# Kernel optimization log

Measured on AMD Instinct MI355X. Metric: run time of the kernel, lower is better.

Reference implementation:

```python
import jax, jax.numpy as jnp
import numpy as np
from jax import lax

Q = 512   # number of FSA states
S = 64    # alphabet size
B = 64    # batch of sequences
T = 256   # sequence length (fixed / padded)


def setup_inputs() -> dict:
    key = jax.random.key(0)
    k_a, k_i, k_f, k_x = jax.random.split(key, 4)
    # Log-space weights centered at -log(Q) so exp(A) ~ 1/Q and the real-semiring
    # forward recursion stays numerically O(1) over T steps.
    A = (-jnp.log(Q) + 0.01 * jax.random.normal(k_a, (Q, S, Q))).astype(jnp.float32)
    init = (-jnp.log(Q) + 0.01 * jax.random.normal(k_i, (Q,))).astype(jnp.float32)
    final = (0.01 * jax.random.normal(k_f, (Q,))).astype(jnp.float32)
    xs = jax.random.randint(k_x, (B, T), 0, S, dtype=jnp.int32)
    return {"A": A, "init": init, "final": final, "xs": xs}


def reference(A, init, final, xs):
    # Weighted-FSA forward algorithm in the real semiring.
    # A: log-space transition weights (Q, S, Q); exp -> positive weights.
    # alpha_t[q] = sum_{q'} exp(A)[q, x_t, q'] * alpha_{t-1}[q']
    A_exp = jnp.exp(A)                       # (Q, S, Q)
    A_sym = jnp.transpose(A_exp, (1, 0, 2))  # (S, Q, Q) for symbol-indexed gather
    b = xs.shape[0]
    alpha0 = jnp.broadcast_to(jnp.exp(init), (b, A.shape[0]))  # (B, Q)

    def step(alpha, x_t):
        # x_t: (B,) symbols at this timestep; gather per-symbol transition matrices
        A_x = A_sym[x_t]                                  # (B, Q, Q)
        alpha = jnp.einsum('bij,bj->bi', A_x, alpha)      # batched matvec
        return alpha, None

    alpha_T, _ = lax.scan(step, alpha0, xs.T)  # scan over time: xs.T is (T, B)
    # Terminate with final weights, return per-sequence log-likelihood (B,)
    return jnp.log(alpha_T @ jnp.exp(final))
```

## Files before the change

### kernel.cpp

```cpp
#include <hip/hip_runtime.h>

#define QN 512
#define SN 64
#define BN 64
#define TN 256
#define GS 4

typedef unsigned long long ull;

#if defined(__has_builtin)
#if __has_builtin(__builtin_amdgcn_sdot4)
#define SDOT4(a, b, c) __builtin_amdgcn_sdot4((a), (b), (c), false)
#endif
#endif
#ifndef SDOT4
static __device__ __forceinline__ int sdot4_sw(int a, int b, int c) {
    c += (int)(signed char)(a)       * (int)(signed char)(b);
    c += (int)(signed char)(a >> 8)  * (int)(signed char)(b >> 8);
    c += (int)(signed char)(a >> 16) * (int)(signed char)(b >> 16);
    c += (int)(signed char)(a >> 24) * (int)(signed char)(b >> 24);
    return c;
}
#define SDOT4(a, b, c) sdot4_sw((a), (b), (c))
#endif

#define NIB_LO(x) ((((x) & 0x0F0F0F0F) ^ 0x08080808) - 0x08080808)
#define NIB_HI(x) (((((x) >> 4) & 0x0F0F0F0F) ^ 0x08080808) - 0x08080808)

static __device__ __forceinline__ float wave_sum(float v) {
    #pragma unroll
    for (int o = 32; o > 0; o >>= 1) v += __shfl_xor(v, o, 64);
    return v;
}
static __device__ __forceinline__ float wave_max(float v) {
    #pragma unroll
    for (int o = 32; o > 0; o >>= 1) v = fmaxf(v, __shfl_xor(v, o, 64));
    return v;
}

static __device__ __forceinline__ void barrier_lds(void) {
    __builtin_amdgcn_s_waitcnt(0xC07F);
    __builtin_amdgcn_s_barrier();
}

static __device__ __forceinline__ void st_tag(ull* p, ull v) {
    __hip_atomic_store(p, v, __ATOMIC_RELAXED, __HIP_MEMORY_SCOPE_AGENT);
}
static __device__ __forceinline__ ull ld_tag(const ull* p) {
    return __hip_atomic_load(p, __ATOMIC_RELAXED, __HIP_MEMORY_SCOPE_AGENT);
}

#define POLL_GUARD (1 << 20)

__global__ __launch_bounds__(256) void k_minmax(const float* __restrict__ A,
                                                unsigned* __restrict__ smax) {
    const int s  = blockIdx.x >> 3;
    const int i0 = (blockIdx.x & 7) * 64;
    const int tl = threadIdx.x & 127;
    const int rh = threadIdx.x >> 7;
    float mx = -1e30f, mn = 1e30f;
    for (int ro = 0; ro < 64; ro += 2) {
        const int i = i0 + ro + rh;
        float4 a4 = ((const float4*)A)[(size_t)(i * 64 + s) * 128 + tl];
        mx = fmaxf(mx, fmaxf(fmaxf(a4.x, a4.y), fmaxf(a4.z, a4.w)));
        mn = fminf(mn, fminf(fminf(a4.x, a4.y), fminf(a4.z, a4.w)));
    }
    mx = wave_max(mx);
    mn = -wave_max(-mn);
    if ((threadIdx.x & 63) == 0) {
        const float c = 1.0f / 512.0f;
        float se = fmaxf(expf(mx) - c, c - expf(mn));
        atomicMax(&smax[s], __float_as_uint(se));
    }
}

__global__ __launch_bounds__(256) void k_quant(const float* __restrict__ A,
                                               const unsigned* __restrict__ smax,
                                               int* __restrict__ Epk,
                                               float* __restrict__ ES,
                                               float* __restrict__ CS) {
    __shared__ int tile[64][129];
    __shared__ float fsumC[64][4];
    const int s  = blockIdx.x >> 3;
    const int i0 = (blockIdx.x & 7) * 64;
    const float se  = __uint_as_float(smax[s]);
    const float inv = se > 0.0f ? 7.0f / se : 0.0f;
    const float c = 1.0f / 512.0f;
    const int tl = threadIdx.x & 127;
    const int rh = threadIdx.x >> 7;
    if (threadIdx.x < 256) ((float*)fsumC)[threadIdx.x] = 0.0f;
    __syncthreads();
    for (int ro = 0; ro < 64; ro += 2) {
        const int r = ro + rh;
        const int i = i0 + r;
        float4 a4 = ((const float4*)A)[(size_t)(i * 64 + s) * 128 + tl];
        const float e0 = expf(a4.x) - c, e1 = expf(a4.y) - c;
        const float e2 = expf(a4.z) - c, e3 = expf(a4.w) - c;
        int q0 = (int)rintf(fminf(fmaxf(e0 * inv, -7.0f), 7.0f));
        int q1 = (int)rintf(fminf(fmaxf(e1 * inv, -7.0f), 7.0f));
        int q2 = (int)rintf(fminf(fmaxf(e2 * inv, -7.0f), 7.0f));
        int q3 = (int)rintf(fminf(fmaxf(e3 * inv, -7.0f), 7.0f));
        tile[r][tl] = (q0 & 255) | ((q1 & 255) << 8) | ((q2 & 255) << 16) | ((q3 & 255) << 24);
        float gs = e0 + e1 + e2 + e3;
        #pragma unroll
        for (int o = 16; o > 0; o >>= 1) gs += __shfl_xor(gs, o, 64);
        if ((threadIdx.x & 31) == 0) atomicAdd(&fsumC[r][tl >> 5], gs);
    }
    __syncthreads();
    if (threadIdx.x < 256) {
        const int r = threadIdx.x >> 2, gg = threadIdx.x & 3;
        CS[((size_t)(s * GS + gg) << 9) + i0 + r] = fsumC[r][gg];
    }
    if (threadIdx.x < 64) {
        const int r = threadIdx.x;
        ES[(s << 9) + i0 + r] = (fsumC[r][0] + fsumC[r][1]) + (fsumC[r][2] + fsumC[r][3]);
    }
    const int il = threadIdx.x & 63;
    const int jg = threadIdx.x >> 6;
    for (int jo = 0; jo < 4; ++jo) {
        const int j32 = jg * 4 + jo;
        int4 v;
        v.x = (tile[il][8 * j32 + 0] & 0x0F0F0F0F) | ((tile[il][8 * j32 + 4] & 0x0F0F0F0F) << 4);
        v.y = (tile[il][8 * j32 + 1] & 0x0F0F0F0F) | ((tile[il][8 * j32 + 5] & 0x0F0F0F0F) << 4);
        v.z = (tile[il][8 * j32 + 2] & 0x0F0F0F0F) | ((tile[il][8 * j32 + 6] & 0x0F0F0F0F) << 4);
        v.w = (tile[il][8 * j32 + 3] & 0x0F0F0F0F) | ((tile[il][8 * j32 + 7] & 0x0F0F0F0F) << 4);
        ((int4*)Epk)[((size_t)(s * 16 + j32) * 512) + i0 + il] = v;
    }
}

__global__ __launch_bounds__(1024) void k_fsa(const int* __restrict__ Epk,
                                              const float* __restrict__ ES,
                                              const float* __restrict__ CS,
                                              const unsigned* __restrict__ smax,
                                              const float* __restrict__ init_w,
                                              const float* __restrict__ fin_w,
                                              const int* __restrict__ xs,
                                              ull* __restrict__ ax,
                                              float* __restrict__ out) {
    __shared__ __align__(16) int qa[2][QN / 4];
    __shared__ __align__(16) int qloc[QN / 16];
    __shared__ int   xs_l[TN];
    __shared__ float wsum[8];
    __shared__ float sws[8];
    __shared__ float se_l[SN];
    __shared__ float mb[2];

    const int t    = threadIdx.x;
    const int b    = blockIdx.x & (BN - 1);
    const int g    = blockIdx.x >> 6;
    const int lane = t & 63, wave = t >> 6;
    const int tr   = t & 3;
    const int lr   = t >> 2;
    const int irow = (g << 7) + lr;
    const int u    = t - 512;

    if (t < TN) xs_l[t] = xs[b * TN + t];
    if (t < SN) se_l[t] = __uint_as_float(smax[t]) * (0.125f / 889.0f);

    const float c  = 1.0f / 512.0f;
    const float Kq = 0.125f;

    const int4* __restrict__ Epb = (const int4*)Epk;
    int4 eR[4], eC[4];
    float ESv = 0.0f, CSv = 0.0f;
    float av = 0.0f;

    if (t < 512) {
        const int s0 = xs[b * TN], s1 = xs[b * TN + 1];
        const int4* EpR = Epb + (size_t)(s0 * 16 + tr * 4) * 512 + irow;
        const int4* EpC = Epb + (size_t)(s1 * 16 + g * 4) * 512 + t;
        #pragma unroll
        for (int k = 0; k < 4; ++k) { eR[k] = EpR[(size_t)k * 512]; eC[k] = EpC[(size_t)k * 512]; }
        if (tr == 0) ESv = ES[(s0 << 9) + irow];
        CSv = CS[((size_t)(s1 * GS + g) << 9) + t];
    } else {
        av = expf(init_w[u]);
        float ws = wave_sum(av);
        if (lane == 0) wsum[wave - 8] = ws;
    }
    barrier_lds();
    if (t >= 512) {
        float m0 = 0.0f;
        #pragma unroll
        for (int w = 0; w < 8; ++w) m0 += wsum[w];
        const float mu     = m0 * (1.0f / 512.0f);
        const float inv_sa = 127.0f / (Kq * mu);
        const int q = (int)rintf(fminf(fmaxf((av - mu) * inv_sa, -127.0f), 127.0f));
        ((char*)qa)[u] = (char)q;
        if (u == 0) mb[0] = m0;
    }
    barrier_lds();

    for (int k = 0; k < TN / 2; ++k) {
        const int par = k & 1;
        float mu = 0.0f;
        if (t < 512) {
            const int sR  = xs_l[2 * k];
            const int sRn = xs_l[(2 * k + 2) & (TN - 1)];
            const float mm = mb[par];
            mu = mm * (1.0f / 512.0f);
            const int4* qp   = (const int4*)qa[par];
            const int4* EpRn = Epb + (size_t)(sRn * 16 + tr * 4) * 512 + irow;
            int a0 = 0, a1 = 0, a2 = 0, a3 = 0;
            #pragma unroll
            for (int k4 = 0; k4 < 4; ++k4) {
                const int4 E4 = eR[k4];
                eR[k4] = EpRn[(size_t)k4 * 512];
                const int4 qlo = qp[2 * (4 * tr + k4) + 0];
                const int4 qhi = qp[2 * (4 * tr + k4) + 1];
                a0 = SDOT4(NIB_LO(E4.x), qlo.x, a0);
                a1 = SDOT4(NIB_HI(E4.x), qhi.x, a1);
                a2 = SDOT4(NIB_LO(E4.y), qlo.y, a2);
                a3 = SDOT4(NIB_HI(E4.y), qhi.y, a3);
                a0 = SDOT4(NIB_LO(E4.z), qlo.z, a0);
                a1 = SDOT4(NIB_HI(E4.z), qhi.z, a1);
                a2 = SDOT4(NIB_LO(E4.w), qlo.w, a2);
                a3 = SDOT4(NIB_HI(E4.w), qhi.w, a3);
            }
            __builtin_amdgcn_sched_barrier(0);
            int acc = (a0 + a1) + (a2 + a3);
            acc += __shfl_xor(acc, 1, 64);
            acc += __shfl_xor(acc, 2, 64);
            float outv = 0.0f;
            if (tr == 0) {
                outv = c * mm + mu * (ESv + se_l[sR] * (float)acc);
                ESv = ES[(sRn << 9) + irow];
                const float inv_sa = 127.0f / (Kq * mu);
                const int q8 = (int)rintf(fminf(fmaxf((outv - mu) * inv_sa, -127.0f), 127.0f));
                ((char*)qloc)[lr] = (char)q8;
            }
            float ws = wave_sum(outv);
            if (lane == 0) sws[wave] = ws;
        }
        barrier_lds();

        if (t < 512) {
            const int sC  = xs_l[2 * k + 1];
            const int sCn = xs_l[(2 * k + 3) & (TN - 1)];
            float Sg = 0.0f;
            #pragma unroll
            for (int w = 0; w < 8; ++w) Sg += sws[w];
            const int4* qc   = (const int4*)qloc;
            const int4* EpCn = Epb + (size_t)(sCn * 16 + g * 4) * 512 + t;
            int a0 = 0, a1 = 0, a2 = 0, a3 = 0;
            #pragma unroll
            for (int k4 = 0; k4 < 4; ++k4) {
                const int4 E4 = eC[k4];
                eC[k4] = EpCn[(size_t)k4 * 512];
                const int4 ql = qc[2 * k4 + 0];
                const int4 qh = qc[2 * k4 + 1];
                a0 = SDOT4(NIB_LO(E4.x), ql.x, a0);
                a1 = SDOT4(NIB_HI(E4.x), qh.x, a1);
                a2 = SDOT4(NIB_LO(E4.y), ql.y, a2);
                a3 = SDOT4(NIB_HI(E4.y), qh.y, a3);
                a0 = SDOT4(NIB_LO(E4.z), ql.z, a0);
                a1 = SDOT4(NIB_HI(E4.z), qh.z, a1);
                a2 = SDOT4(NIB_LO(E4.w), ql.w, a2);
                a3 = SDOT4(NIB_HI(E4.w), qh.w, a3);
            }
            __builtin_amdgcn_sched_barrier(0);
            const int accC = (a0 + a1) + (a2 + a3);
            const float y = c * Sg + mu * (CSv + se_l[sC] * (float)accC);
            CSv = CS[((size_t)(sCn * GS + g) << 9) + t];
            st_tag(ax + ((size_t)((par ^ 1) * BN + b) * GS + g) * QN + t,
                   ((ull)(unsigned)(k + 1) << 32) | (ull)__float_as_uint(y));
        } else {
            const unsigned want = (unsigned)(k + 1);
            const ull* ap = ax + (size_t)((par ^ 1) * BN + b) * GS * QN + u;
            ull w0 = ld_tag(ap + 0 * QN);
            ull w1 = ld_tag(ap + 1 * QN);
            ull w2 = ld_tag(ap + 2 * QN);
            ull w3 = ld_tag(ap + 3 * QN);
            int gd = 0;
            while ((((unsigned)(w0 >> 32) < want) | ((unsigned)(w1 >> 32) < want) |
                    ((unsigned)(w2 >> 32) < want) | ((unsigned)(w3 >> 32) < want)) &&
                   ++gd < POLL_GUARD) {
                __builtin_amdgcn_s_sleep(1);
                w0 = ld_tag(ap + 0 * QN);
                w1 = ld_tag(ap + 1 * QN);
                w2 = ld_tag(ap + 2 * QN);
                w3 = ld_tag(ap + 3 * QN);
            }
            av = (__uint_as_float((unsigned)w0) + __uint_as_float((unsigned)w1)) +
                 (__uint_as_float((unsigned)w2) + __uint_as_float((unsigned)w3));
            float ws = wave_sum(av);
            if (lane == 0) wsum[wave - 8] = ws;
        }
        barrier_lds();

        if (t >= 512) {
            float m = 0.0f;
            #pragma unroll
            for (int w = 0; w < 8; ++w) m += wsum[w];
            const float mu2    = m * (1.0f / 512.0f);
            const float inv_sa = 127.0f / (Kq * mu2);
            const int q = (int)rintf(fminf(fmaxf((av - mu2) * inv_sa, -127.0f), 127.0f));
            ((char*)qa)[(par ^ 1) * QN + u] = (char)q;
            if (u == 0) mb[par ^ 1] = m;
        }
        barrier_lds();
    }

    {
        float v = 0.0f;
        if (t >= 512) {
            v = av * expf(fin_w[u]);
            float ws = wave_sum(v);
            if (lane == 0) wsum[wave - 8] = ws;
        }
        barrier_lds();
        if (g == 0 && t == 512) {
            float tot = 0.0f;
            #pragma unroll
            for (int w = 0; w < 8; ++w) tot += wsum[w];
            out[b] = logf(tot);
        }
    }
}

extern "C" void kernel_launch(void* const* d_in, const int* in_sizes, int n_in,
                              void* d_out, int out_size, void* d_ws, size_t ws_size,
                              hipStream_t stream) {
    const float* A      = (const float*)d_in[0];
    const float* init_w = (const float*)d_in[1];
    const float* fin_w  = (const float*)d_in[2];
    const int*   xs     = (const int*)d_in[3];
    float* out = (float*)d_out;

    char* ws = (char*)d_ws;
    int*      Epk  = (int*)ws;
    float*    ES   = (float*)(ws + (8u << 20));
    float*    CS   = (float*)(ws + (8u << 20) + (128u << 10));
    unsigned* smax = (unsigned*)(ws + (8u << 20) + (640u << 10));
    ull*      ax   = (ull*)(ws + (8u << 20) + (641u << 10));

    hipMemsetAsync(smax, 0, (1u << 10) + (2u << 20), stream);
    k_minmax<<<512, 256, 0, stream>>>(A, smax);
    k_quant<<<512, 256, 0, stream>>>(A, smax, Epk, ES, CS);
    k_fsa<<<GS * BN, 1024, 0, stream>>>(Epk, ES, CS, smax, init_w, fin_w, xs, ax, out);
}
```

Measured before the change: 651.7 us.

## Split each sequence's FSA recursion across eight workgroups instead of four

Doubles the number of cooperating workgroups per sequence (GS 4→8), so each block handles 64 rows and a 64-column slice of the quantized transition matrix. This halves the per-block register preload and the dot-product work per step. In exchange, each step now needs eight tagged partial vectors to be polled and summed, an extra shuffle stage is added, and twice as many blocks (512) must be co-resident for the inter-block spin synchronization to make progress. Workspace offsets and the memset size are enlarged to fit the larger partial-sum buffer.

```diff
diff --git a/kernel.cpp b/kernel.cpp
--- a/kernel.cpp
+++ b/kernel.cpp
@@ -4,7 +4,7 @@
 #define SN 64
 #define BN 64
 #define TN 256
-#define GS 4
+#define GS 8
 
 typedef unsigned long long ull;
 
@@ -80,7 +80,7 @@
                                                float* __restrict__ ES,
                                                float* __restrict__ CS) {
     __shared__ int tile[64][129];
-    __shared__ float fsumC[64][4];
+    __shared__ float fsumC[64][GS];
     const int s  = blockIdx.x >> 3;
     const int i0 = (blockIdx.x & 7) * 64;
     const float se  = __uint_as_float(smax[s]);
@@ -88,7 +88,10 @@
     const float c = 1.0f / 512.0f;
     const int tl = threadIdx.x & 127;
     const int rh = threadIdx.x >> 7;
-    if (threadIdx.x < 256) ((float*)fsumC)[threadIdx.x] = 0.0f;
+    if (threadIdx.x < 256) {
+        ((float*)fsumC)[threadIdx.x] = 0.0f;
+        ((float*)fsumC)[256 + threadIdx.x] = 0.0f;
+    }
     __syncthreads();
     for (int ro = 0; ro < 64; ro += 2) {
         const int r = ro + rh;
@@ -103,17 +106,24 @@
         tile[r][tl] = (q0 & 255) | ((q1 & 255) << 8) | ((q2 & 255) << 16) | ((q3 & 255) << 24);
         float gs = e0 + e1 + e2 + e3;
         #pragma unroll
-        for (int o = 16; o > 0; o >>= 1) gs += __shfl_xor(gs, o, 64);
-        if ((threadIdx.x & 31) == 0) atomicAdd(&fsumC[r][tl >> 5], gs);
+        for (int o = 8; o > 0; o >>= 1) gs += __shfl_xor(gs, o, 64);
+        if ((threadIdx.x & 15) == 0) atomicAdd(&fsumC[r][tl >> 4], gs);
     }
     __syncthreads();
     if (threadIdx.x < 256) {
-        const int r = threadIdx.x >> 2, gg = threadIdx.x & 3;
-        CS[((size_t)(s * GS + gg) << 9) + i0 + r] = fsumC[r][gg];
+        #pragma unroll
+        for (int h = 0; h < 2; ++h) {
+            const int idx = threadIdx.x + 256 * h;
+            const int r = idx >> 3, gg = idx & 7;
+            CS[((size_t)(s * GS + gg) << 9) + i0 + r] = fsumC[r][gg];
+        }
     }
     if (threadIdx.x < 64) {
         const int r = threadIdx.x;
-        ES[(s << 9) + i0 + r] = (fsumC[r][0] + fsumC[r][1]) + (fsumC[r][2] + fsumC[r][3]);
+        float es = 0.0f;
+        #pragma unroll
+        for (int gg = 0; gg < GS; ++gg) es += fsumC[r][gg];
+        ES[(s << 9) + i0 + r] = es;
     }
     const int il = threadIdx.x & 63;
     const int jg = threadIdx.x >> 6;
@@ -128,17 +138,17 @@
     }
 }
 
-__global__ __launch_bounds__(1024) void k_fsa(const int* __restrict__ Epk,
-                                              const float* __restrict__ ES,
-                                              const float* __restrict__ CS,
-                                              const unsigned* __restrict__ smax,
-                                              const float* __restrict__ init_w,
-                                              const float* __restrict__ fin_w,
-                                              const int* __restrict__ xs,
-                                              ull* __restrict__ ax,
-                                              float* __restrict__ out) {
+__global__ __launch_bounds__(1024, 8) void k_fsa(const int* __restrict__ Epk,
+                                                 const float* __restrict__ ES,
+                                                 const float* __restrict__ CS,
+                                                 const unsigned* __restrict__ smax,
+                                                 const float* __restrict__ init_w,
+                                                 const float* __restrict__ fin_w,
+                                                 const int* __restrict__ xs,
+                                                 ull* __restrict__ ax,
+                                                 float* __restrict__ out) {
     __shared__ __align__(16) int qa[2][QN / 4];
-    __shared__ __align__(16) int qloc[QN / 16];
+    __shared__ __align__(16) int qloc[16];
     __shared__ int   xs_l[TN];
     __shared__ float wsum[8];
     __shared__ float sws[8];
@@ -149,9 +159,9 @@
     const int b    = blockIdx.x & (BN - 1);
     const int g    = blockIdx.x >> 6;
     const int lane = t & 63, wave = t >> 6;
-    const int tr   = t & 3;
-    const int lr   = t >> 2;
-    const int irow = (g << 7) + lr;
+    const int tr   = t & 7;
+    const int lr   = t >> 3;
+    const int irow = (g << 6) + lr;
     const int u    = t - 512;
 
     if (t < TN) xs_l[t] = xs[b * TN + t];
@@ -161,16 +171,16 @@
     const float Kq = 0.125f;
 
     const int4* __restrict__ Epb = (const int4*)Epk;
-    int4 eR[4], eC[4];
+    int4 eR[2], eC[2];
     float ESv = 0.0f, CSv = 0.0f;
     float av = 0.0f;
 
     if (t < 512) {
         const int s0 = xs[b * TN], s1 = xs[b * TN + 1];
-        const int4* EpR = Epb + (size_t)(s0 * 16 + tr * 4) * 512 + irow;
-        const int4* EpC = Epb + (size_t)(s1 * 16 + g * 4) * 512 + t;
-        #pragma unroll
-        for (int k = 0; k < 4; ++k) { eR[k] = EpR[(size_t)k * 512]; eC[k] = EpC[(size_t)k * 512]; }
+        const int4* EpR = Epb + (size_t)(s0 * 16 + tr * 2) * 512 + irow;
+        const int4* EpC = Epb + (size_t)(s1 * 16 + g * 2) * 512 + t;
+        #pragma unroll
+        for (int k = 0; k < 2; ++k) { eR[k] = EpR[(size_t)k * 512]; eC[k] = EpC[(size_t)k * 512]; }
         if (tr == 0) ESv = ES[(s0 << 9) + irow];
         CSv = CS[((size_t)(s1 * GS + g) << 9) + t];
     } else {
@@ -200,14 +210,14 @@
             const float mm = mb[par];
             mu = mm * (1.0f / 512.0f);
             const int4* qp   = (const int4*)qa[par];
-            const int4* EpRn = Epb + (size_t)(sRn * 16 + tr * 4) * 512 + irow;
+            const int4* EpRn = Epb + (size_t)(sRn * 16 + tr * 2) * 512 + irow;
             int a0 = 0, a1 = 0, a2 = 0, a3 = 0;
             #pragma unroll
-            for (int k4 = 0; k4 < 4; ++k4) {
+            for (int k4 = 0; k4 < 2; ++k4) {
                 const int4 E4 = eR[k4];
                 eR[k4] = EpRn[(size_t)k4 * 512];
-                const int4 qlo = qp[2 * (4 * tr + k4) + 0];
-                const int4 qhi = qp[2 * (4 * tr + k4) + 1];
+                const int4 qlo = qp[2 * (2 * tr + k4) + 0];
+                const int4 qhi = qp[2 * (2 * tr + k4) + 1];
                 a0 = SDOT4(NIB_LO(E4.x), qlo.x, a0);
                 a1 = SDOT4(NIB_HI(E4.x), qhi.x, a1);
                 a2 = SDOT4(NIB_LO(E4.y), qlo.y, a2);
@@ -221,6 +231,7 @@
             int acc = (a0 + a1) + (a2 + a3);
             acc += __shfl_xor(acc, 1, 64);
             acc += __shfl_xor(acc, 2, 64);
+            acc += __shfl_xor(acc, 4, 64);
             float outv = 0.0f;
             if (tr == 0) {
                 outv = c * mm + mu * (ESv + se_l[sR] * (float)acc);
@@ -241,10 +252,10 @@
             #pragma unroll
             for (int w = 0; w < 8; ++w) Sg += sws[w];
             const int4* qc   = (const int4*)qloc;
-            const int4* EpCn = Epb + (size_t)(sCn * 16 + g * 4) * 512 + t;
+            const int4* EpCn = Epb + (size_t)(sCn * 16 + g * 2) * 512 + t;
             int a0 = 0, a1 = 0, a2 = 0, a3 = 0;
             #pragma unroll
-            for (int k4 = 0; k4 < 4; ++k4) {
+            for (int k4 = 0; k4 < 2; ++k4) {
                 const int4 E4 = eC[k4];
                 eC[k4] = EpCn[(size_t)k4 * 512];
                 const int4 ql = qc[2 * k4 + 0];
@@ -267,22 +278,26 @@
         } else {
             const unsigned want = (unsigned)(k + 1);
             const ull* ap = ax + (size_t)((par ^ 1) * BN + b) * GS * QN + u;
-            ull w0 = ld_tag(ap + 0 * QN);
-            ull w1 = ld_tag(ap + 1 * QN);
-            ull w2 = ld_tag(ap + 2 * QN);
-            ull w3 = ld_tag(ap + 3 * QN);
+            ull w0 = ld_tag(ap + 0 * QN), w1 = ld_tag(ap + 1 * QN);
+            ull w2 = ld_tag(ap + 2 * QN), w3 = ld_tag(ap + 3 * QN);
+            ull w4 = ld_tag(ap + 4 * QN), w5 = ld_tag(ap + 5 * QN);
+            ull w6 = ld_tag(ap + 6 * QN), w7 = ld_tag(ap + 7 * QN);
             int gd = 0;
             while ((((unsigned)(w0 >> 32) < want) | ((unsigned)(w1 >> 32) < want) |
-                    ((unsigned)(w2 >> 32) < want) | ((unsigned)(w3 >> 32) < want)) &&
+                    ((unsigned)(w2 >> 32) < want) | ((unsigned)(w3 >> 32) < want) |
+                    ((unsigned)(w4 >> 32) < want) | ((unsigned)(w5 >> 32) < want) |
+                    ((unsigned)(w6 >> 32) < want) | ((unsigned)(w7 >> 32) < want)) &&
                    ++gd < POLL_GUARD) {
                 __builtin_amdgcn_s_sleep(1);
-                w0 = ld_tag(ap + 0 * QN);
-                w1 = ld_tag(ap + 1 * QN);
-                w2 = ld_tag(ap + 2 * QN);
-                w3 = ld_tag(ap + 3 * QN);
+                w0 = ld_tag(ap + 0 * QN); w1 = ld_tag(ap + 1 * QN);
+                w2 = ld_tag(ap + 2 * QN); w3 = ld_tag(ap + 3 * QN);
+                w4 = ld_tag(ap + 4 * QN); w5 = ld_tag(ap + 5 * QN);
+                w6 = ld_tag(ap + 6 * QN); w7 = ld_tag(ap + 7 * QN);
             }
-            av = (__uint_as_float((unsigned)w0) + __uint_as_float((unsigned)w1)) +
-                 (__uint_as_float((unsigned)w2) + __uint_as_float((unsigned)w3));
+            av = ((__uint_as_float((unsigned)w0) + __uint_as_float((unsigned)w1)) +
+                  (__uint_as_float((unsigned)w2) + __uint_as_float((unsigned)w3))) +
+                 ((__uint_as_float((unsigned)w4) + __uint_as_float((unsigned)w5)) +
+                  (__uint_as_float((unsigned)w6) + __uint_as_float((unsigned)w7)));
             float ws = wave_sum(av);
             if (lane == 0) wsum[wave - 8] = ws;
         }
@@ -331,10 +346,10 @@
     int*      Epk  = (int*)ws;
     float*    ES   = (float*)(ws + (8u << 20));
     float*    CS   = (float*)(ws + (8u << 20) + (128u << 10));
-    unsigned* smax = (unsigned*)(ws + (8u << 20) + (640u << 10));
-    ull*      ax   = (ull*)(ws + (8u << 20) + (641u << 10));
-
-    hipMemsetAsync(smax, 0, (1u << 10) + (2u << 20), stream);
+    unsigned* smax = (unsigned*)(ws + (9u << 20) + (128u << 10));
+    ull*      ax   = (ull*)(ws + (9u << 20) + (129u << 10));
+
+    hipMemsetAsync(smax, 0, (1u << 10) + (4u << 20), stream);
     k_minmax<<<512, 256, 0, stream>>>(A, smax);
     k_quant<<<512, 256, 0, stream>>>(A, smax, Epk, ES, CS);
     k_fsa<<<GS * BN, 1024, 0, stream>>>(Epk, ES, CS, smax, init_w, fin_w, xs, ax, out);
```

After: 2.009 ms. 208% more time.

## Fuse minmax and quantize kernels with per-symbol inter-block counter sync

Applied to the files above, without the earlier changes.

Merges the min/max scan and quantization kernels into one launch. The eight blocks sharing a symbol now combine their scale through a global atomic counter and spin-wait, which removes a kernel launch and its boundary. It also remaps the FSA block index so the four groups for one sequence are adjacent. The spin-wait assumes all eight cooperating blocks are resident at once (512 blocks of 256 threads should fit), and it adds polling latency.

```diff
diff --git a/kernel.cpp b/kernel.cpp
--- a/kernel.cpp
+++ b/kernel.cpp
@@ -52,12 +52,22 @@
 
 #define POLL_GUARD (1 << 20)
 
-__global__ __launch_bounds__(256) void k_minmax(const float* __restrict__ A,
-                                                unsigned* __restrict__ smax) {
+__global__ __launch_bounds__(256) void k_prep(const float* __restrict__ A,
+                                              unsigned* __restrict__ smax,
+                                              unsigned* __restrict__ cnt,
+                                              int* __restrict__ Epk,
+                                              float* __restrict__ ES,
+                                              float* __restrict__ CS) {
+    __shared__ int tile[64][129];
+    __shared__ float fsumC[64][GS];
+    __shared__ float wmx[4], wmn[4];
+    __shared__ float se_sh;
     const int s  = blockIdx.x >> 3;
     const int i0 = (blockIdx.x & 7) * 64;
     const int tl = threadIdx.x & 127;
     const int rh = threadIdx.x >> 7;
+    const float c = 1.0f / 512.0f;
+
     float mx = -1e30f, mn = 1e30f;
     for (int ro = 0; ro < 64; ro += 2) {
         const int i = i0 + ro + rh;
@@ -67,29 +77,29 @@
     }
     mx = wave_max(mx);
     mn = -wave_max(-mn);
-    if ((threadIdx.x & 63) == 0) {
-        const float c = 1.0f / 512.0f;
-        float se = fmaxf(expf(mx) - c, c - expf(mn));
-        atomicMax(&smax[s], __float_as_uint(se));
-    }
-}
-
-__global__ __launch_bounds__(256) void k_quant(const float* __restrict__ A,
-                                               const unsigned* __restrict__ smax,
-                                               int* __restrict__ Epk,
-                                               float* __restrict__ ES,
-                                               float* __restrict__ CS) {
-    __shared__ int tile[64][129];
-    __shared__ float fsumC[64][4];
-    const int s  = blockIdx.x >> 3;
-    const int i0 = (blockIdx.x & 7) * 64;
-    const float se  = __uint_as_float(smax[s]);
-    const float inv = se > 0.0f ? 7.0f / se : 0.0f;
-    const float c = 1.0f / 512.0f;
-    const int tl = threadIdx.x & 127;
-    const int rh = threadIdx.x >> 7;
+    if ((threadIdx.x & 63) == 0) { wmx[threadIdx.x >> 6] = mx; wmn[threadIdx.x >> 6] = mn; }
     if (threadIdx.x < 256) ((float*)fsumC)[threadIdx.x] = 0.0f;
     __syncthreads();
+    if (threadIdx.x == 0) {
+        const float bmx = fmaxf(fmaxf(wmx[0], wmx[1]), fmaxf(wmx[2], wmx[3]));
+        const float bmn = fminf(fminf(wmn[0], wmn[1]), fminf(wmn[2], wmn[3]));
+        const float se = fmaxf(expf(bmx) - c, c - expf(bmn));
+        atomicMax(&smax[s], __float_as_uint(se));
+        __threadfence();
+        atomicAdd(&cnt[s], 1u);
+        unsigned v = __hip_atomic_load(&cnt[s], __ATOMIC_ACQUIRE, __HIP_MEMORY_SCOPE_AGENT);
+        int gd = 0;
+        while (v < 8u && ++gd < POLL_GUARD) {
+            __builtin_amdgcn_s_sleep(1);
+            v = __hip_atomic_load(&cnt[s], __ATOMIC_ACQUIRE, __HIP_MEMORY_SCOPE_AGENT);
+        }
+        se_sh = __uint_as_float(
+            __hip_atomic_load(&smax[s], __ATOMIC_RELAXED, __HIP_MEMORY_SCOPE_AGENT));
+    }
+    __syncthreads();
+    const float se  = se_sh;
+    const float inv = se > 0.0f ? 7.0f / se : 0.0f;
+
     for (int ro = 0; ro < 64; ro += 2) {
         const int r = ro + rh;
         const int i = i0 + r;
@@ -146,8 +156,8 @@
     __shared__ float mb[2];
 
     const int t    = threadIdx.x;
-    const int b    = blockIdx.x & (BN - 1);
-    const int g    = blockIdx.x >> 6;
+    const int b    = blockIdx.x >> 2;
+    const int g    = blockIdx.x & (GS - 1);
     const int lane = t & 63, wave = t >> 6;
     const int tr   = t & 3;
     const int lr   = t >> 2;
@@ -332,10 +342,10 @@
     float*    ES   = (float*)(ws + (8u << 20));
     float*    CS   = (float*)(ws + (8u << 20) + (128u << 10));
     unsigned* smax = (unsigned*)(ws + (8u << 20) + (640u << 10));
-    ull*      ax   = (ull*)(ws + (8u << 20) + (641u << 10));
-
-    hipMemsetAsync(smax, 0, (1u << 10) + (2u << 20), stream);
-    k_minmax<<<512, 256, 0, stream>>>(A, smax);
-    k_quant<<<512, 256, 0, stream>>>(A, smax, Epk, ES, CS);
+    unsigned* cnt  = (unsigned*)(ws + (8u << 20) + (641u << 10));
+    ull*      ax   = (ull*)(ws + (8u << 20) + (642u << 10));
+
+    hipMemsetAsync(smax, 0, (2u << 10) + (2u << 20), stream);
+    k_prep<<<512, 256, 0, stream>>>(A, smax, cnt, Epk, ES, CS);
     k_fsa<<<GS * BN, 1024, 0, stream>>>(Epk, ES, CS, smax, init_w, fin_w, xs, ax, out);
 }
```

After: 669.5 us. +2.7%, slower.
